# Optimization experiments

Hardware: AMD Instinct MI355X
Metric: run time of the kernel (lower is better)

The kernel has to match this reference:

```python
import jax, jax.numpy as jnp
import numpy as np

B, S, D = 1024, 256, 256  # batch, n_class, feature dim (g = n_component = 1)


def setup_inputs() -> dict:
    key = jax.random.key(0)
    k1, k2, k3 = jax.random.split(key, 3)
    x = jax.random.normal(k1, (B, D), dtype=jnp.float32)
    mu_p = jax.random.normal(k2, (S, 1, D), dtype=jnp.float32)
    sigma_p = jax.random.normal(k3, (S, 1, D, D), dtype=jnp.float32)
    return {"x": x, "mu_p": mu_p, "sigma_p": sigma_p}


def _log_probs(x, mu_p, sigma_p):
    sp = sigma_p[:, 0]            # (S, D, D), component index g=0
    mu = mu_p[:, 0]               # (S, D)
    # parameter_enforcing: m = sigma_p^T @ sigma_p (PSD);
    # mean of (real) eigenvalues of m == trace(m)/D, so the ridge term is
    # 0.01 * (trace(m)/D) * I, making sigma symmetric positive definite.
    m = jnp.einsum('skd,ske->sde', sp, sp)                      # (S, D, D)
    ridge = 0.01 * (jnp.trace(m, axis1=-2, axis2=-1) / D)       # (S,)
    sigma = m + ridge[:, None, None] * jnp.eye(D, dtype=m.dtype)
    # MVN log_prob via Cholesky: logdet = 2*sum(log diag L),
    # maha = || L^{-1} (x - mu) ||^2
    L = jnp.linalg.cholesky(sigma)                              # (S, D, D)
    logdet = 2.0 * jnp.sum(jnp.log(jnp.diagonal(L, axis1=-2, axis2=-1)), -1)  # (S,)
    diff = x[None, :, :] - mu[:, None, :]                       # (S, B, D)
    # batched triangular solve per class: y = L^{-1} diff^T -> (S, D, B)
    y = jax.vmap(lambda Ls, ds: jax.scipy.linalg.solve_triangular(Ls, ds.T, lower=True))(L, diff)
    maha = jnp.sum(y * y, axis=1)                               # (S, B)
    log2pi = jnp.log(2.0 * jnp.pi).astype(x.dtype)
    logp = -0.5 * (D * log2pi + logdet[:, None] + maha)         # (S, B)
    return logp.T                                               # (B, S)


def reference(x, mu_p, sigma_p):
    return _log_probs(x, mu_p, sigma_p)
```

## Files before the change

### kernel.cpp

```cpp
#include <hip/hip_runtime.h>
#include <math.h>


#define LOG2PI_D 470.4965290007924f

typedef __attribute__((ext_vector_type(8))) short bf16x8;
typedef __attribute__((ext_vector_type(4))) float f32x4;

__device__ __forceinline__ unsigned bf16rtn(float f) {
  unsigned u = __float_as_uint(f);
  return (u + 0x7FFFu + ((u >> 16) & 1u)) >> 16;
}
__device__ __forceinline__ unsigned packhl(float v) {
  unsigned h = bf16rtn(v);
  float hf = __uint_as_float(h << 16);
  unsigned l = bf16rtn(v - hf);
  return (h << 16) | l;
}

__global__ __launch_bounds__(256) void k_gram(const float* __restrict__ sp,
                                              float* __restrict__ L,
                                              float* __restrict__ ridge_out) {
  __shared__ unsigned Hb[4 * 128 * 20];
  unsigned* AH = Hb;
  unsigned* AL = Hb + 128 * 20;
  unsigned* BH = Hb + 2 * 128 * 20;
  unsigned* BL = Hb + 3 * 128 * 20;
  int p = blockIdx.y, s = blockIdx.x;
  int bi = (p ? 128 : 0), bj = (p == 2 ? 128 : 0);
  const float* A = sp + (size_t)s * 65536;
  float* C = L + (size_t)s * 65536;
  int tid = threadIdx.x, w = tid >> 6, lane = tid & 63;
  int q = lane >> 4, n = lane & 15;
  int mt_[2] = {w, 7 - w};
  f32x4 acc[2][8] = {};
  int c = tid & 127, g = tid >> 7;

  float va[16], vb[16];
#pragma unroll
  for (int u = 0; u < 16; ++u) {
    va[u] = A[(size_t)(g * 16 + u) * 256 + bi + c];
    if (p == 1) vb[u] = A[(size_t)(g * 16 + u) * 256 + bj + c];
  }

  for (int ks = 0; ks < 8; ++ks) {
    __syncthreads();
    {
      unsigned hw[8], lw[8];
#pragma unroll
      for (int m = 0; m < 8; ++m) {
        float v0 = va[2 * m], v1 = va[2 * m + 1];
        unsigned h0 = bf16rtn(v0), h1 = bf16rtn(v1);
        float r0 = v0 - __uint_as_float(h0 << 16);
        float r1 = v1 - __uint_as_float(h1 << 16);
        hw[m] = h0 | (h1 << 16);
        lw[m] = bf16rtn(r0) | (bf16rtn(r1) << 16);
      }
      *(uint4*)&AH[c * 20 + g * 8] = make_uint4(hw[0], hw[1], hw[2], hw[3]);
      *(uint4*)&AH[c * 20 + g * 8 + 4] = make_uint4(hw[4], hw[5], hw[6], hw[7]);
      *(uint4*)&AL[c * 20 + g * 8] = make_uint4(lw[0], lw[1], lw[2], lw[3]);
      *(uint4*)&AL[c * 20 + g * 8 + 4] = make_uint4(lw[4], lw[5], lw[6], lw[7]);
      if (p == 1) {
#pragma unroll
        for (int m = 0; m < 8; ++m) {
          float v0 = vb[2 * m], v1 = vb[2 * m + 1];
          unsigned h0 = bf16rtn(v0), h1 = bf16rtn(v1);
          float r0 = v0 - __uint_as_float(h0 << 16);
          float r1 = v1 - __uint_as_float(h1 << 16);
          hw[m] = h0 | (h1 << 16);
          lw[m] = bf16rtn(r0) | (bf16rtn(r1) << 16);
        }
        *(uint4*)&BH[c * 20 + g * 8] = make_uint4(hw[0], hw[1], hw[2], hw[3]);
        *(uint4*)&BH[c * 20 + g * 8 + 4] = make_uint4(hw[4], hw[5], hw[6], hw[7]);
        *(uint4*)&BL[c * 20 + g * 8] = make_uint4(lw[0], lw[1], lw[2], lw[3]);
        *(uint4*)&BL[c * 20 + g * 8 + 4] = make_uint4(lw[4], lw[5], lw[6], lw[7]);
      }
    }
    __syncthreads();
    if (ks < 7) {
      int r0g = (ks + 1) * 32 + g * 16;
#pragma unroll
      for (int u = 0; u < 16; ++u) {
        va[u] = A[(size_t)(r0g + u) * 256 + bi + c];
        if (p == 1) vb[u] = A[(size_t)(r0g + u) * 256 + bj + c];
      }
    }
    const unsigned* TBH = (p == 1) ? BH : AH;
    const unsigned* TBL = (p == 1) ? BL : AL;
    bf16x8 Ah[2], Al[2];
#pragma unroll
    for (int t = 0; t < 2; ++t) {
      int col = mt_[t] * 16 + n;
      Ah[t] = *(const bf16x8*)&AH[col * 20 + q * 4];
      Al[t] = *(const bf16x8*)&AL[col * 20 + q * 4];
    }
    int ntmax = (p == 1) ? 8 : (8 - w);
    for (int nt = 0; nt < ntmax; ++nt) {
      bf16x8 bh = *(const bf16x8*)&TBH[(nt * 16 + n) * 20 + q * 4];
      bf16x8 bl = *(const bf16x8*)&TBL[(nt * 16 + n) * 20 + q * 4];
#pragma unroll
      for (int t = 0; t < 2; ++t) {
        if (p == 1 || nt <= mt_[t]) {
          acc[t][nt] = __builtin_amdgcn_mfma_f32_16x16x32_bf16(Ah[t], bh, acc[t][nt], 0, 0, 0);
          acc[t][nt] = __builtin_amdgcn_mfma_f32_16x16x32_bf16(Ah[t], bl, acc[t][nt], 0, 0, 0);
          acc[t][nt] = __builtin_amdgcn_mfma_f32_16x16x32_bf16(Al[t], bh, acc[t][nt], 0, 0, 0);
        }
      }
    }
  }
  if (p != 1) {
    float dsum = 0.f;
#pragma unroll
    for (int t = 0; t < 2; ++t) {
      if ((n >> 2) == q) dsum += acc[t][mt_[t]][n & 3];
    }
    dsum += __shfl_down(dsum, 32, 64);
    dsum += __shfl_down(dsum, 16, 64);
    dsum += __shfl_down(dsum, 8, 64);
    dsum += __shfl_down(dsum, 4, 64);
    dsum += __shfl_down(dsum, 2, 64);
    dsum += __shfl_down(dsum, 1, 64);
    if (lane == 0) atomicAdd(&ridge_out[s], dsum * (0.01f / 256.0f));
  }
  float* slab = (float*)Hb;
  for (int t = 0; t < 2; ++t) {
    __syncthreads();
#pragma unroll
    for (int nt = 0; nt < 8; ++nt)
#pragma unroll
      for (int r = 0; r < 4; ++r)
        slab[w * 2048 + (q * 4 + r) * 128 + nt * 16 + n] = acc[t][nt][r];
    __syncthreads();
#pragma unroll
    for (int it = 0; it < 8; ++it) {
      int idx = tid + it * 256;
      int row = idx >> 5, c4 = idx & 31;
      int wsrc = row >> 4, r16 = row & 15;
      int rt = t ? (7 - wsrc) : wsrc;
      if (p == 1 || (c4 >> 2) <= rt) {
        int d = bi + rt * 16 + r16;
        *(float4*)(C + (size_t)d * 256 + bj + c4 * 4) =
            *(float4*)&slab[wsrc * 2048 + r16 * 128 + c4 * 4];
      }
    }
  }
}

__global__ __launch_bounds__(256) void k_factor(float* __restrict__ L,
                                                const float* __restrict__ ridge_buf) {
  extern __shared__ float lds[];
  float* P = lds;
  float* W = lds + 64 * 68;
  float* WT = lds + 2 * 64 * 68;
  float* T = lds + 3 * 64 * 68;
  int s = blockIdx.x;
  float* M = L + (size_t)s * 65536;
  unsigned* M32 = (unsigned*)M;
  int tid = threadIdx.x;
  int k4 = tid & 15, rb = tid >> 4;
  int ty = tid >> 4, tx = tid & 15;
  float ridge = ridge_buf[s];

  for (int kb = 0; kb < 4; ++kb) {
    int base = kb * 64;
    __syncthreads();
    for (int r = rb; r < 64; r += 16)
      *(float4*)&P[r * 68 + k4 * 4] = *(const float4*)(M + (size_t)(base + r) * 256 + base + k4 * 4);
    __syncthreads();
    if (tid < 64) P[tid * 68 + tid] += ridge;
    __syncthreads();
    {
      int eo = tid & 63, ro = tid >> 6;
      for (int cb = 0; cb < 16; ++cb) {
        int c0 = cb * 4;
        float g00 = P[c0 * 68 + c0];
        float g10 = P[(c0 + 1) * 68 + c0], g11 = P[(c0 + 1) * 68 + c0 + 1];
        float g20 = P[(c0 + 2) * 68 + c0], g21 = P[(c0 + 2) * 68 + c0 + 1],
              g22 = P[(c0 + 2) * 68 + c0 + 2];
        float g30 = P[(c0 + 3) * 68 + c0], g31 = P[(c0 + 3) * 68 + c0 + 1],
              g32 = P[(c0 + 3) * 68 + c0 + 2], g33 = P[(c0 + 3) * 68 + c0 + 3];
        float l00 = sqrtf(g00), r0 = 1.f / l00;
        float l10 = g10 * r0, l20 = g20 * r0, l30 = g30 * r0;
        float l11 = sqrtf(g11 - l10 * l10), r1 = 1.f / l11;
        float l21 = (g21 - l20 * l10) * r1, l31 = (g31 - l30 * l10) * r1;
        float l22 = sqrtf(g22 - l20 * l20 - l21 * l21), r2 = 1.f / l22;
        float l32 = (g32 - l30 * l20 - l31 * l21) * r2;
        float l33 = sqrtf(g33 - l30 * l30 - l31 * l31 - l32 * l32), r3 = 1.f / l33;
        int e = c0 + 4 + eo;
        if (e < 64) {
          float p0 = P[e * 68 + c0], p1 = P[e * 68 + c0 + 1];
          float p2 = P[e * 68 + c0 + 2], p3 = P[e * 68 + c0 + 3];
          float le0 = p0 * r0;
          float le1 = (p1 - le0 * l10) * r1;
          float le2 = (p2 - le0 * l20 - le1 * l21) * r2;
          float le3 = (p3 - le0 * l30 - le1 * l31 - le2 * l32) * r3;
          for (int r = c0 + 4 + ro; r < 64; r += 4) {
            float q0 = P[r * 68 + c0], q1 = P[r * 68 + c0 + 1];
            float q2 = P[r * 68 + c0 + 2], q3 = P[r * 68 + c0 + 3];
            float lr0 = q0 * r0;
            float lr1 = (q1 - lr0 * l10) * r1;
            float lr2 = (q2 - lr0 * l20 - lr1 * l21) * r2;
            float lr3 = (q3 - lr0 * l30 - lr1 * l31 - lr2 * l32) * r3;
            P[r * 68 + e] -= lr0 * le0 + lr1 * le1 + lr2 * le2 + lr3 * le3;
          }
        }
        __syncthreads();
      }
    }
    {
      int cb = tid >> 4, lane16 = tid & 15;
      int c0 = cb * 4;
      float g00 = P[c0 * 68 + c0];
      float g10 = P[(c0 + 1) * 68 + c0], g11 = P[(c0 + 1) * 68 + c0 + 1];
      float g20 = P[(c0 + 2) * 68 + c0], g21 = P[(c0 + 2) * 68 + c0 + 1],
            g22 = P[(c0 + 2) * 68 + c0 + 2];
      float g30 = P[(c0 + 3) * 68 + c0], g31 = P[(c0 + 3) * 68 + c0 + 1],
            g32 = P[(c0 + 3) * 68 + c0 + 2], g33 = P[(c0 + 3) * 68 + c0 + 3];
      float l00 = sqrtf(g00), r0 = 1.f / l00;
      float l10 = g10 * r0, l20 = g20 * r0, l30 = g30 * r0;
      float l11 = sqrtf(g11 - l10 * l10), r1 = 1.f / l11;
      float l21 = (g21 - l20 * l10) * r1, l31 = (g31 - l30 * l10) * r1;
      float l22 = sqrtf(g22 - l20 * l20 - l21 * l21), r2 = 1.f / l22;
      float l32 = (g32 - l30 * l20 - l31 * l21) * r2;
      float l33 = sqrtf(g33 - l30 * l30 - l31 * l31 - l32 * l32), r3 = 1.f / l33;
      float vals[4][4];
      int rows[4], nr = 0;
      for (int r = c0 + lane16; r < 64; r += 16) {
        int i = r - c0;
        if (i == 0) { vals[nr][0] = l00; vals[nr][1] = 0; vals[nr][2] = 0; vals[nr][3] = 0; }
        else if (i == 1) { vals[nr][0] = l10; vals[nr][1] = l11; vals[nr][2] = 0; vals[nr][3] = 0; }
        else if (i == 2) { vals[nr][0] = l20; vals[nr][1] = l21; vals[nr][2] = l22; vals[nr][3] = 0; }
        else if (i == 3) { vals[nr][0] = l30; vals[nr][1] = l31; vals[nr][2] = l32; vals[nr][3] = l33; }
        else {
          float q0 = P[r * 68 + c0], q1 = P[r * 68 + c0 + 1];
          float q2 = P[r * 68 + c0 + 2], q3 = P[r * 68 + c0 + 3];
          float lr0 = q0 * r0;
          float lr1 = (q1 - lr0 * l10) * r1;
          float lr2 = (q2 - lr0 * l20 - lr1 * l21) * r2;
          float lr3 = (q3 - lr0 * l30 - lr1 * l31 - lr2 * l32) * r3;
          vals[nr][0] = lr0; vals[nr][1] = lr1; vals[nr][2] = lr2; vals[nr][3] = lr3;
        }
        rows[nr++] = r;
      }
      __syncthreads();
      for (int u = 0; u < nr; ++u) {
        int r = rows[u];
        P[r * 68 + c0] = vals[u][0];
        P[r * 68 + c0 + 1] = vals[u][1];
        P[r * 68 + c0 + 2] = vals[u][2];
        P[r * 68 + c0 + 3] = vals[u][3];
      }
    }
    __syncthreads();
    if (tid < 64) {
      int c = tid;
      int rl = (c < 32) ? 32 : 64;
      for (int r = 0; r < c; ++r) W[r * 68 + c] = 0.f;
      W[c * 68 + c] = 1.0f / P[c * 68 + c];
      for (int r = c + 1; r < rl; ++r) {
        float a = 0.f;
        for (int k = c; k < r; ++k) a += P[r * 68 + k] * W[k * 68 + c];
        W[r * 68 + c] = -a / P[r * 68 + r];
      }
    }
    __syncthreads();
    {
      int r0 = (tid >> 4) * 2, c0 = (tid & 15) * 2;
      float a00 = 0, a01 = 0, a10 = 0, a11 = 0;
      for (int k = 0; k < 32; ++k) {
        float b0 = P[(32 + r0) * 68 + k], b1 = P[(33 + r0) * 68 + k];
        float w0 = W[k * 68 + c0], w1 = W[k * 68 + c0 + 1];
        a00 += b0 * w0; a01 += b0 * w1; a10 += b1 * w0; a11 += b1 * w1;
      }
      T[r0 * 68 + c0] = a00; T[r0 * 68 + c0 + 1] = a01;
      T[(r0 + 1) * 68 + c0] = a10; T[(r0 + 1) * 68 + c0 + 1] = a11;
    }
    __syncthreads();
    {
      int r0 = (tid >> 4) * 2, c0 = (tid & 15) * 2;
      float a00 = 0, a01 = 0, a10 = 0, a11 = 0;
      for (int k = 0; k < 32; ++k) {
        float i0 = W[(32 + r0) * 68 + 32 + k], i1 = W[(33 + r0) * 68 + 32 + k];
        float t0 = T[k * 68 + c0], t1 = T[k * 68 + c0 + 1];
        a00 += i0 * t0; a01 += i0 * t1; a10 += i1 * t0; a11 += i1 * t1;
      }
      W[(32 + r0) * 68 + c0] = -a00; W[(32 + r0) * 68 + c0 + 1] = -a01;
      W[(33 + r0) * 68 + c0] = -a10; W[(33 + r0) * 68 + c0 + 1] = -a11;
    }
    __syncthreads();
    for (int c = rb; c < 64; c += 16) {
      float4 v = *(float4*)&W[c * 68 + k4 * 4];
      WT[(k4 * 4 + 0) * 68 + c] = v.x;
      WT[(k4 * 4 + 1) * 68 + c] = v.y;
      WT[(k4 * 4 + 2) * 68 + c] = v.z;
      WT[(k4 * 4 + 3) * 68 + c] = v.w;
    }
    __syncthreads();
    for (int r = rb; r < 64; r += 16)
      *(float4*)(M + (size_t)(base + r) * 256 + base + k4 * 4) = *(float4*)&W[r * 68 + k4 * 4];
    int nrt = 3 - kb;
    for (int rt = 0; rt < nrt; ++rt) {
      int g0 = base + 64 + rt * 64;
      __syncthreads();
      for (int r = rb; r < 64; r += 16) {
        float4 v = *(const float4*)(M + (size_t)(g0 + r) * 256 + base + k4 * 4);
        T[(k4 * 4 + 0) * 68 + r] = v.x;
        T[(k4 * 4 + 1) * 68 + r] = v.y;
        T[(k4 * 4 + 2) * 68 + r] = v.z;
        T[(k4 * 4 + 3) * 68 + r] = v.w;
      }
      __syncthreads();
      float acc[4][4] = {};
      for (int k = 0; k < 64; ++k) {
        float a[4], b[4];
        *(float4*)a = *(float4*)&T[k * 68 + ty * 4];
        *(float4*)b = *(float4*)&WT[k * 68 + tx * 4];
#pragma unroll
        for (int i = 0; i < 4; ++i)
#pragma unroll
          for (int j = 0; j < 4; ++j) acc[i][j] += a[i] * b[j];
      }
      __syncthreads();
#pragma unroll
      for (int i = 0; i < 4; ++i)
        *(float4*)(M + (size_t)(g0 + ty * 4 + i) * 256 + base + tx * 4) =
            make_float4(acc[i][0], acc[i][1], acc[i][2], acc[i][3]);
#pragma unroll
      for (int i = 0; i < 4; ++i)
#pragma unroll
        for (int j = 0; j < 4; ++j) T[(tx * 4 + j) * 68 + ty * 4 + i] = acc[i][j];
      __syncthreads();
      for (int r = rb; r < 64; r += 16)
        *(float4*)(M + (size_t)(base + r) * 256 + g0 + k4 * 4) = *(float4*)&T[r * 68 + k4 * 4];
    }
    for (int ti = kb + 1; ti < 4; ++ti) {
      for (int tj = kb + 1; tj <= ti; ++tj) {
        __syncthreads();
        for (int k = rb; k < 64; k += 16) {
          *(float4*)&P[k * 68 + k4 * 4] =
              *(const float4*)(M + (size_t)(base + k) * 256 + ti * 64 + k4 * 4);
          *(float4*)&W[k * 68 + k4 * 4] =
              *(const float4*)(M + (size_t)(base + k) * 256 + tj * 64 + k4 * 4);
        }
        float acc[4][4];
#pragma unroll
        for (int i = 0; i < 4; ++i)
          *(float4*)&acc[i][0] =
              *(const float4*)(M + (size_t)(ti * 64 + ty * 4 + i) * 256 + tj * 64 + tx * 4);
        __syncthreads();
        for (int k = 0; k < 64; ++k) {
          float a[4], b[4];
          *(float4*)a = *(float4*)&P[k * 68 + ty * 4];
          *(float4*)b = *(float4*)&W[k * 68 + tx * 4];
#pragma unroll
          for (int i = 0; i < 4; ++i)
#pragma unroll
            for (int j = 0; j < 4; ++j) acc[i][j] -= a[i] * b[j];
        }
#pragma unroll
        for (int i = 0; i < 4; ++i)
          *(float4*)(M + (size_t)(ti * 64 + ty * 4 + i) * 256 + tj * 64 + tx * 4) =
              make_float4(acc[i][0], acc[i][1], acc[i][2], acc[i][3]);
      }
    }
  }

  {
    float* Bcol = lds;
    float* LW = lds + 3 * 64 * 68;
    float* Cs = LW + 64 * 68;
    for (int j = 0; j < 3; ++j) {
      __syncthreads();
      for (int r = rb; r < 64; r += 16)
        *(float4*)&Bcol[r * 68 + k4 * 4] =
            *(const float4*)(M + (size_t)(j * 64 + r) * 256 + j * 64 + k4 * 4);
      __syncthreads();

      for (int i = j + 1; i < 4; ++i) {
        float acc[4][4] = {};
        for (int kk = j; kk < i; ++kk) {
          __syncthreads();
          for (int k = rb; k < 64; k += 16)
            *(float4*)&LW[k * 68 + k4 * 4] =
                *(const float4*)(M + (size_t)(kk * 64 + k) * 256 + i * 64 + k4 * 4);
          __syncthreads();
          float* Bk = Bcol + (kk - j) * 64 * 68;
#pragma unroll 4
          for (int k = 0; k < 64; ++k) {
            float a[4], b[4];
            *(float4*)a = *(float4*)&LW[k * 68 + ty * 4];
            *(float4*)b = *(float4*)&Bk[k * 68 + tx * 4];
#pragma unroll
            for (int r = 0; r < 4; ++r)
#pragma unroll
              for (int cc = 0; cc < 4; ++cc) acc[r][cc] += a[r] * b[cc];
          }
        }
        __syncthreads();
#pragma unroll
        for (int r = 0; r < 4; ++r)
          *(float4*)&Cs[(ty * 4 + r) * 68 + tx * 4] =
              make_float4(acc[r][0], acc[r][1], acc[r][2], acc[r][3]);
        for (int r = rb; r < 64; r += 16) {
          float4 v = *(const float4*)(M + (size_t)(i * 64 + r) * 256 + i * 64 + k4 * 4);
          LW[(k4 * 4 + 0) * 68 + r] = v.x;
          LW[(k4 * 4 + 1) * 68 + r] = v.y;
          LW[(k4 * 4 + 2) * 68 + r] = v.z;
          LW[(k4 * 4 + 3) * 68 + r] = v.w;
        }
        __syncthreads();
        float d[4][4] = {};
#pragma unroll 4
        for (int k = 0; k < 64; ++k) {
          float a[4], b[4];
          *(float4*)a = *(float4*)&LW[k * 68 + ty * 4];
          *(float4*)b = *(float4*)&Cs[k * 68 + tx * 4];
#pragma unroll
          for (int r = 0; r < 4; ++r)
#pragma unroll
            for (int cc = 0; cc < 4; ++cc) d[r][cc] -= a[r] * b[cc];
        }
        float* Bi = Bcol + (i - j) * 64 * 68;
#pragma unroll
        for (int r = 0; r < 4; ++r) {
          if (i < 3)
            *(float4*)&Bi[(ty * 4 + r) * 68 + tx * 4] =
                make_float4(d[r][0], d[r][1], d[r][2], d[r][3]);
          uint4 pu;
          pu.x = packhl(d[r][0]); pu.y = packhl(d[r][1]);
          pu.z = packhl(d[r][2]); pu.w = packhl(d[r][3]);
          *(uint4*)(M32 + (size_t)(i * 64 + ty * 4 + r) * 256 + j * 64 + tx * 4) = pu;
        }
        __syncthreads();
      }
    }
  }
}

__global__ __launch_bounds__(512) void k_maha(const float* __restrict__ x,
                                              const float* __restrict__ mu_p,
                                              const float* __restrict__ Lw,
                                              float* __restrict__ out) {
  __shared__ __align__(16) short Bh[128 * 40];
  __shared__ __align__(16) short Bl[128 * 40];
  __shared__ float Red[1025];
  int s = blockIdx.x, b0 = blockIdx.y * 128;
  const float* Mf = Lw + (size_t)s * 65536;
  const unsigned* M32 = (const unsigned*)Mf;
  int tid = threadIdx.x, w = tid >> 6, lane = tid & 63;
  int q = lane >> 4, n = lane & 15;
  int mt_[2] = {w, 15 - w};
  f32x4 acc[2][8] = {};

  for (int ks = 0; ks < 8; ++ks) {
    __syncthreads();
    {
      int b = tid >> 2, q8 = tid & 3;
      const float* xp = x + (size_t)(b0 + b) * 256 + ks * 32 + q8 * 8;
      const float* mp = mu_p + (size_t)s * 256 + ks * 32 + q8 * 8;
      float4 xa = ((const float4*)xp)[0], xb = ((const float4*)xp)[1];
      float4 ma = ((const float4*)mp)[0], mb = ((const float4*)mp)[1];
      float dv[8] = {xa.x - ma.x, xa.y - ma.y, xa.z - ma.z, xa.w - ma.w,
                     xb.x - mb.x, xb.y - mb.y, xb.z - mb.z, xb.w - mb.w};
      unsigned h[8], l[8];
#pragma unroll
      for (int jj = 0; jj < 8; ++jj) {
        h[jj] = bf16rtn(dv[jj]);
        float hf = __uint_as_float(h[jj] << 16);
        l[jj] = bf16rtn(dv[jj] - hf);
      }
      *(uint4*)&Bh[b * 40 + q8 * 8] =
          make_uint4(h[0] | (h[1] << 16), h[2] | (h[3] << 16),
                     h[4] | (h[5] << 16), h[6] | (h[7] << 16));
      *(uint4*)&Bl[b * 40 + q8 * 8] =
          make_uint4(l[0] | (l[1] << 16), l[2] | (l[3] << 16),
                     l[4] | (l[5] << 16), l[6] | (l[7] << 16));
    }
    __syncthreads();
    bf16x8 Ah[2], Al[2];
    bool act[2];
#pragma unroll
    for (int t = 0; t < 2; ++t) {
      int mt = mt_[t];
      act[t] = ks < ((mt + 2) >> 1);
      if (act[t]) {
        const unsigned* ap = M32 + (size_t)(mt * 16 + n) * 256 + ks * 32 + q * 8;
        uint4 u0 = *(const uint4*)ap;
        uint4 u1 = *(const uint4*)(ap + 4);
        unsigned uu[8] = {u0.x, u0.y, u0.z, u0.w, u1.x, u1.y, u1.z, u1.w};
        if ((ks >> 1) == (mt >> 2)) {
#pragma unroll
          for (int jj = 0; jj < 8; ++jj) {
            float f = __uint_as_float(uu[jj]);
            unsigned hh = bf16rtn(f);
            float hf = __uint_as_float(hh << 16);
            Ah[t][jj] = (short)hh;
            Al[t][jj] = (short)bf16rtn(f - hf);
          }
        } else {
#pragma unroll
          for (int jj = 0; jj < 8; ++jj) {
            Ah[t][jj] = (short)(uu[jj] >> 16);
            Al[t][jj] = (short)(uu[jj] & 0xffffu);
          }
        }
      }
    }
#pragma unroll
    for (int bsub = 0; bsub < 8; ++bsub) {
      bf16x8 bh = *(const bf16x8*)&Bh[(bsub * 16 + n) * 40 + q * 8];
      bf16x8 bl = *(const bf16x8*)&Bl[(bsub * 16 + n) * 40 + q * 8];
#pragma unroll
      for (int t = 0; t < 2; ++t) {
        if (act[t]) {
          acc[t][bsub] = __builtin_amdgcn_mfma_f32_16x16x32_bf16(Ah[t], bh, acc[t][bsub], 0, 0, 0);
          acc[t][bsub] = __builtin_amdgcn_mfma_f32_16x16x32_bf16(Ah[t], bl, acc[t][bsub], 0, 0, 0);
          acc[t][bsub] = __builtin_amdgcn_mfma_f32_16x16x32_bf16(Al[t], bh, acc[t][bsub], 0, 0, 0);
        }
      }
    }
  }
#pragma unroll
  for (int bsub = 0; bsub < 8; ++bsub) {
    float v = 0.f;
#pragma unroll
    for (int t = 0; t < 2; ++t)
#pragma unroll
      for (int r = 0; r < 4; ++r) v += acc[t][bsub][r] * acc[t][bsub][r];
    v += __shfl_xor(v, 16, 64);
    v += __shfl_xor(v, 32, 64);
    if (lane < 16) Red[w * 128 + bsub * 16 + lane] = v;
  }
  if (w == 0) {
    float ld = 0.f;
#pragma unroll
    for (int c = 0; c < 4; ++c)
      ld += logf(Mf[(size_t)(c * 64 + lane) * 256 + c * 64 + lane]);
    ld += __shfl_down(ld, 32, 64);
    ld += __shfl_down(ld, 16, 64);
    ld += __shfl_down(ld, 8, 64);
    ld += __shfl_down(ld, 4, 64);
    ld += __shfl_down(ld, 2, 64);
    ld += __shfl_down(ld, 1, 64);
    if (lane == 0) Red[1024] = ld;
  }
  __syncthreads();
  if (tid < 128) {
    float mh = 0.f;
#pragma unroll
    for (int w2 = 0; w2 < 8; ++w2) mh += Red[w2 * 128 + tid];
    out[(size_t)(b0 + tid) * 256 + s] = -0.5f * (LOG2PI_D - 2.0f * Red[1024] + mh);
  }
}

extern "C" void kernel_launch(void* const* d_in, const int* in_sizes, int n_in,
                              void* d_out, int out_size, void* d_ws, size_t ws_size,
                              hipStream_t stream) {
  const float* x = (const float*)d_in[0];
  const float* mu = (const float*)d_in[1];
  const float* sp = (const float*)d_in[2];
  float* out = (float*)d_out;
  float* L = (float*)d_ws;

  const int fact_lds = 5 * 64 * 68 * 4;
  (void)hipFuncSetAttribute((const void*)k_factor,
                            hipFuncAttributeMaxDynamicSharedMemorySize, fact_lds);

  k_gram<<<dim3(256, 3), 256, 0, stream>>>(sp, L, out);
  k_factor<<<256, 256, fact_lds, stream>>>(L, out);
  k_maha<<<dim3(256, 8), 512, 0, stream>>>(x, mu, L, out);
}
```

Measured before the change: 654.7 us.

## Double factor kernel block size and process two trailing tiles concurrently

Raises k_factor to 512 threads per block. The two thread halves now process pairs of panel and trailing-update tiles in parallel, using an extra LDS buffer. The diagonal-block triangular inverse changes from a serial per-column loop on 64 threads to a blocked 4-row forward substitution driven by a 256-thread partial-sum step. The intent is to raise per-block parallelism in the serial Cholesky phase, at the cost of idle threads in some phases, extra barriers and higher register pressure.

New measurement: 614.7 us. 6.1% less time.

```diff
diff --git a/kernel.cpp b/kernel.cpp
--- a/kernel.cpp
+++ b/kernel.cpp
@@ -146,19 +146,19 @@
   }
 }
 
-__global__ __launch_bounds__(256) void k_factor(float* __restrict__ L,
+__global__ __launch_bounds__(512) void k_factor(float* __restrict__ L,
                                                 const float* __restrict__ ridge_buf) {
   extern __shared__ float lds[];
   float* P = lds;
   float* W = lds + 64 * 68;
   float* WT = lds + 2 * 64 * 68;
   float* T = lds + 3 * 64 * 68;
+  float* T2 = lds + 4 * 64 * 68;
   int s = blockIdx.x;
   float* M = L + (size_t)s * 65536;
   unsigned* M32 = (unsigned*)M;
   int tid = threadIdx.x;
   int k4 = tid & 15, rb = tid >> 4;
-  int ty = tid >> 4, tx = tid & 15;
   float ridge = ridge_buf[s];
 
   for (int kb = 0; kb < 4; ++kb) {
@@ -194,7 +194,7 @@
           float le1 = (p1 - le0 * l10) * r1;
           float le2 = (p2 - le0 * l20 - le1 * l21) * r2;
           float le3 = (p3 - le0 * l30 - le1 * l31 - le2 * l32) * r3;
-          for (int r = c0 + 4 + ro; r < 64; r += 4) {
+          for (int r = c0 + 4 + ro; r < 64; r += 8) {
             float q0 = P[r * 68 + c0], q1 = P[r * 68 + c0 + 1];
             float q2 = P[r * 68 + c0 + 2], q3 = P[r * 68 + c0 + 3];
             float lr0 = q0 * r0;
@@ -210,84 +210,85 @@
     {
       int cb = tid >> 4, lane16 = tid & 15;
       int c0 = cb * 4;
-      float g00 = P[c0 * 68 + c0];
-      float g10 = P[(c0 + 1) * 68 + c0], g11 = P[(c0 + 1) * 68 + c0 + 1];
-      float g20 = P[(c0 + 2) * 68 + c0], g21 = P[(c0 + 2) * 68 + c0 + 1],
-            g22 = P[(c0 + 2) * 68 + c0 + 2];
-      float g30 = P[(c0 + 3) * 68 + c0], g31 = P[(c0 + 3) * 68 + c0 + 1],
-            g32 = P[(c0 + 3) * 68 + c0 + 2], g33 = P[(c0 + 3) * 68 + c0 + 3];
-      float l00 = sqrtf(g00), r0 = 1.f / l00;
-      float l10 = g10 * r0, l20 = g20 * r0, l30 = g30 * r0;
-      float l11 = sqrtf(g11 - l10 * l10), r1 = 1.f / l11;
-      float l21 = (g21 - l20 * l10) * r1, l31 = (g31 - l30 * l10) * r1;
-      float l22 = sqrtf(g22 - l20 * l20 - l21 * l21), r2 = 1.f / l22;
-      float l32 = (g32 - l30 * l20 - l31 * l21) * r2;
-      float l33 = sqrtf(g33 - l30 * l30 - l31 * l31 - l32 * l32), r3 = 1.f / l33;
       float vals[4][4];
       int rows[4], nr = 0;
-      for (int r = c0 + lane16; r < 64; r += 16) {
-        int i = r - c0;
-        if (i == 0) { vals[nr][0] = l00; vals[nr][1] = 0; vals[nr][2] = 0; vals[nr][3] = 0; }
-        else if (i == 1) { vals[nr][0] = l10; vals[nr][1] = l11; vals[nr][2] = 0; vals[nr][3] = 0; }
-        else if (i == 2) { vals[nr][0] = l20; vals[nr][1] = l21; vals[nr][2] = l22; vals[nr][3] = 0; }
-        else if (i == 3) { vals[nr][0] = l30; vals[nr][1] = l31; vals[nr][2] = l32; vals[nr][3] = l33; }
-        else {
-          float q0 = P[r * 68 + c0], q1 = P[r * 68 + c0 + 1];
-          float q2 = P[r * 68 + c0 + 2], q3 = P[r * 68 + c0 + 3];
-          float lr0 = q0 * r0;
-          float lr1 = (q1 - lr0 * l10) * r1;
-          float lr2 = (q2 - lr0 * l20 - lr1 * l21) * r2;
-          float lr3 = (q3 - lr0 * l30 - lr1 * l31 - lr2 * l32) * r3;
-          vals[nr][0] = lr0; vals[nr][1] = lr1; vals[nr][2] = lr2; vals[nr][3] = lr3;
-        }
-        rows[nr++] = r;
-      }
-      __syncthreads();
-      for (int u = 0; u < nr; ++u) {
-        int r = rows[u];
-        P[r * 68 + c0] = vals[u][0];
-        P[r * 68 + c0 + 1] = vals[u][1];
-        P[r * 68 + c0 + 2] = vals[u][2];
-        P[r * 68 + c0 + 3] = vals[u][3];
-      }
-    }
-    __syncthreads();
-    if (tid < 64) {
-      int c = tid;
-      int rl = (c < 32) ? 32 : 64;
-      for (int r = 0; r < c; ++r) W[r * 68 + c] = 0.f;
-      W[c * 68 + c] = 1.0f / P[c * 68 + c];
-      for (int r = c + 1; r < rl; ++r) {
-        float a = 0.f;
-        for (int k = c; k < r; ++k) a += P[r * 68 + k] * W[k * 68 + c];
-        W[r * 68 + c] = -a / P[r * 68 + r];
-      }
-    }
-    __syncthreads();
-    {
-      int r0 = (tid >> 4) * 2, c0 = (tid & 15) * 2;
-      float a00 = 0, a01 = 0, a10 = 0, a11 = 0;
-      for (int k = 0; k < 32; ++k) {
-        float b0 = P[(32 + r0) * 68 + k], b1 = P[(33 + r0) * 68 + k];
-        float w0 = W[k * 68 + c0], w1 = W[k * 68 + c0 + 1];
-        a00 += b0 * w0; a01 += b0 * w1; a10 += b1 * w0; a11 += b1 * w1;
-      }
-      T[r0 * 68 + c0] = a00; T[r0 * 68 + c0 + 1] = a01;
-      T[(r0 + 1) * 68 + c0] = a10; T[(r0 + 1) * 68 + c0 + 1] = a11;
-    }
-    __syncthreads();
-    {
-      int r0 = (tid >> 4) * 2, c0 = (tid & 15) * 2;
-      float a00 = 0, a01 = 0, a10 = 0, a11 = 0;
-      for (int k = 0; k < 32; ++k) {
-        float i0 = W[(32 + r0) * 68 + 32 + k], i1 = W[(33 + r0) * 68 + 32 + k];
-        float t0 = T[k * 68 + c0], t1 = T[k * 68 + c0 + 1];
-        a00 += i0 * t0; a01 += i0 * t1; a10 += i1 * t0; a11 += i1 * t1;
-      }
-      W[(32 + r0) * 68 + c0] = -a00; W[(32 + r0) * 68 + c0 + 1] = -a01;
-      W[(33 + r0) * 68 + c0] = -a10; W[(33 + r0) * 68 + c0 + 1] = -a11;
-    }
-    __syncthreads();
+      if (tid < 256) {
+        float g00 = P[c0 * 68 + c0];
+        float g10 = P[(c0 + 1) * 68 + c0], g11 = P[(c0 + 1) * 68 + c0 + 1];
+        float g20 = P[(c0 + 2) * 68 + c0], g21 = P[(c0 + 2) * 68 + c0 + 1],
+              g22 = P[(c0 + 2) * 68 + c0 + 2];
+        float g30 = P[(c0 + 3) * 68 + c0], g31 = P[(c0 + 3) * 68 + c0 + 1],
+              g32 = P[(c0 + 3) * 68 + c0 + 2], g33 = P[(c0 + 3) * 68 + c0 + 3];
+        float l00 = sqrtf(g00), r0 = 1.f / l00;
+        float l10 = g10 * r0, l20 = g20 * r0, l30 = g30 * r0;
+        float l11 = sqrtf(g11 - l10 * l10), r1 = 1.f / l11;
+        float l21 = (g21 - l20 * l10) * r1, l31 = (g31 - l30 * l10) * r1;
+        float l22 = sqrtf(g22 - l20 * l20 - l21 * l21), r2 = 1.f / l22;
+        float l32 = (g32 - l30 * l20 - l31 * l21) * r2;
+        float l33 = sqrtf(g33 - l30 * l30 - l31 * l31 - l32 * l32), r3 = 1.f / l33;
+        for (int r = c0 + lane16; r < 64; r += 16) {
+          int i = r - c0;
+          if (i == 0) { vals[nr][0] = l00; vals[nr][1] = 0; vals[nr][2] = 0; vals[nr][3] = 0; }
+          else if (i == 1) { vals[nr][0] = l10; vals[nr][1] = l11; vals[nr][2] = 0; vals[nr][3] = 0; }
+          else if (i == 2) { vals[nr][0] = l20; vals[nr][1] = l21; vals[nr][2] = l22; vals[nr][3] = 0; }
+          else if (i == 3) { vals[nr][0] = l30; vals[nr][1] = l31; vals[nr][2] = l32; vals[nr][3] = l33; }
+          else {
+            float q0 = P[r * 68 + c0], q1 = P[r * 68 + c0 + 1];
+            float q2 = P[r * 68 + c0 + 2], q3 = P[r * 68 + c0 + 3];
+            float lr0 = q0 * r0;
+            float lr1 = (q1 - lr0 * l10) * r1;
+            float lr2 = (q2 - lr0 * l20 - lr1 * l21) * r2;
+            float lr3 = (q3 - lr0 * l30 - lr1 * l31 - lr2 * l32) * r3;
+            vals[nr][0] = lr0; vals[nr][1] = lr1; vals[nr][2] = lr2; vals[nr][3] = lr3;
+          }
+          rows[nr++] = r;
+        }
+      }
+      __syncthreads();
+      if (tid < 256) {
+        for (int u = 0; u < nr; ++u) {
+          int r = rows[u];
+          P[r * 68 + c0] = vals[u][0];
+          P[r * 68 + c0 + 1] = vals[u][1];
+          P[r * 68 + c0 + 2] = vals[u][2];
+          P[r * 68 + c0 + 3] = vals[u][3];
+        }
+      }
+    }
+    __syncthreads();
+    for (int idx = tid; idx < 64 * 68; idx += 512) W[idx] = 0.f;
+    __syncthreads();
+    for (int rb4 = 0; rb4 < 16; ++rb4) {
+      int k0 = rb4 * 4;
+      if (tid < 256) {
+        int i = tid >> 6, cc = tid & 63;
+        int row = k0 + i;
+        float ssum = 0.f;
+        for (int k = 0; k < k0; ++k) ssum += P[row * 68 + k] * W[k * 68 + cc];
+        WT[i * 68 + cc] = ssum;
+      }
+      __syncthreads();
+      if (tid < 64) {
+        int cc = tid;
+        float d00 = P[(k0 + 0) * 68 + k0];
+        float d10 = P[(k0 + 1) * 68 + k0], d11 = P[(k0 + 1) * 68 + k0 + 1];
+        float d20 = P[(k0 + 2) * 68 + k0], d21 = P[(k0 + 2) * 68 + k0 + 1],
+              d22 = P[(k0 + 2) * 68 + k0 + 2];
+        float d30 = P[(k0 + 3) * 68 + k0], d31 = P[(k0 + 3) * 68 + k0 + 1],
+              d32 = P[(k0 + 3) * 68 + k0 + 2], d33 = P[(k0 + 3) * 68 + k0 + 3];
+        float e0 = (cc == k0) ? 1.f : 0.f, e1 = (cc == k0 + 1) ? 1.f : 0.f;
+        float e2 = (cc == k0 + 2) ? 1.f : 0.f, e3 = (cc == k0 + 3) ? 1.f : 0.f;
+        float x0 = (e0 - WT[0 * 68 + cc]) / d00;
+        float x1 = (e1 - WT[1 * 68 + cc] - d10 * x0) / d11;
+        float x2 = (e2 - WT[2 * 68 + cc] - d20 * x0 - d21 * x1) / d22;
+        float x3 = (e3 - WT[3 * 68 + cc] - d30 * x0 - d31 * x1 - d32 * x2) / d33;
+        W[(k0 + 0) * 68 + cc] = x0;
+        W[(k0 + 1) * 68 + cc] = x1;
+        W[(k0 + 2) * 68 + cc] = x2;
+        W[(k0 + 3) * 68 + cc] = x3;
+      }
+      __syncthreads();
+    }
     for (int c = rb; c < 64; c += 16) {
       float4 v = *(float4*)&W[c * 68 + k4 * 4];
       WT[(k4 * 4 + 0) * 68 + c] = v.x;
@@ -299,59 +300,92 @@
     for (int r = rb; r < 64; r += 16)
       *(float4*)(M + (size_t)(base + r) * 256 + base + k4 * 4) = *(float4*)&W[r * 68 + k4 * 4];
     int nrt = 3 - kb;
-    for (int rt = 0; rt < nrt; ++rt) {
-      int g0 = base + 64 + rt * 64;
-      __syncthreads();
-      for (int r = rb; r < 64; r += 16) {
-        float4 v = *(const float4*)(M + (size_t)(g0 + r) * 256 + base + k4 * 4);
-        T[(k4 * 4 + 0) * 68 + r] = v.x;
-        T[(k4 * 4 + 1) * 68 + r] = v.y;
-        T[(k4 * 4 + 2) * 68 + r] = v.z;
-        T[(k4 * 4 + 3) * 68 + r] = v.w;
+    for (int rt0 = 0; rt0 < nrt; rt0 += 2) {
+      int pr = tid >> 8, t2 = tid & 255;
+      int my = rt0 + pr;
+      bool act = my < nrt;
+      float* Tb = pr ? T2 : T;
+      int k42 = t2 & 15, rb2 = t2 >> 4;
+      int ty2 = t2 >> 4, tx2 = t2 & 15;
+      int g0 = base + 64 + my * 64;
+      __syncthreads();
+      if (act) {
+        for (int r = rb2; r < 64; r += 16) {
+          float4 v = *(const float4*)(M + (size_t)(g0 + r) * 256 + base + k42 * 4);
+          Tb[(k42 * 4 + 0) * 68 + r] = v.x;
+          Tb[(k42 * 4 + 1) * 68 + r] = v.y;
+          Tb[(k42 * 4 + 2) * 68 + r] = v.z;
+          Tb[(k42 * 4 + 3) * 68 + r] = v.w;
+        }
       }
       __syncthreads();
       float acc[4][4] = {};
-      for (int k = 0; k < 64; ++k) {
-        float a[4], b[4];
-        *(float4*)a = *(float4*)&T[k * 68 + ty * 4];
-        *(float4*)b = *(float4*)&WT[k * 68 + tx * 4];
+      if (act) {
+        for (int k = 0; k < 64; ++k) {
+          float a[4], b[4];
+          *(float4*)a = *(float4*)&Tb[k * 68 + ty2 * 4];
+          *(float4*)b = *(float4*)&WT[k * 68 + tx2 * 4];
+#pragma unroll
+          for (int i = 0; i < 4; ++i)
+#pragma unroll
+            for (int j = 0; j < 4; ++j) acc[i][j] += a[i] * b[j];
+        }
+      }
+      __syncthreads();
+      if (act) {
 #pragma unroll
         for (int i = 0; i < 4; ++i)
-#pragma unroll
-          for (int j = 0; j < 4; ++j) acc[i][j] += a[i] * b[j];
-      }
-      __syncthreads();
-#pragma unroll
-      for (int i = 0; i < 4; ++i)
-        *(float4*)(M + (size_t)(g0 + ty * 4 + i) * 256 + base + tx * 4) =
-            make_float4(acc[i][0], acc[i][1], acc[i][2], acc[i][3]);
-#pragma unroll
-      for (int i = 0; i < 4; ++i)
-#pragma unroll
-        for (int j = 0; j < 4; ++j) T[(tx * 4 + j) * 68 + ty * 4 + i] = acc[i][j];
-      __syncthreads();
-      for (int r = rb; r < 64; r += 16)
-        *(float4*)(M + (size_t)(base + r) * 256 + g0 + k4 * 4) = *(float4*)&T[r * 68 + k4 * 4];
-    }
-    for (int ti = kb + 1; ti < 4; ++ti) {
-      for (int tj = kb + 1; tj <= ti; ++tj) {
-        __syncthreads();
-        for (int k = rb; k < 64; k += 16) {
-          *(float4*)&P[k * 68 + k4 * 4] =
-              *(const float4*)(M + (size_t)(base + k) * 256 + ti * 64 + k4 * 4);
-          *(float4*)&W[k * 68 + k4 * 4] =
-              *(const float4*)(M + (size_t)(base + k) * 256 + tj * 64 + k4 * 4);
-        }
-        float acc[4][4];
+          *(float4*)(M + (size_t)(g0 + ty2 * 4 + i) * 256 + base + tx2 * 4) =
+              make_float4(acc[i][0], acc[i][1], acc[i][2], acc[i][3]);
+#pragma unroll
+        for (int i = 0; i < 4; ++i)
+#pragma unroll
+          for (int j = 0; j < 4; ++j) Tb[(tx2 * 4 + j) * 68 + ty2 * 4 + i] = acc[i][j];
+      }
+      __syncthreads();
+      if (act) {
+        for (int r = rb2; r < 64; r += 16)
+          *(float4*)(M + (size_t)(base + r) * 256 + g0 + k42 * 4) = *(float4*)&Tb[r * 68 + k42 * 4];
+      }
+    }
+    int np = ((3 - kb) * (4 - kb)) / 2;
+    for (int p0 = 0; p0 < np; p0 += 2) {
+      int pr = tid >> 8, t2 = tid & 255;
+      int my = p0 + pr;
+      bool act = my < np;
+      int ti = 1, tj = 1;
+      {
+        int cnt = 0;
+        for (int a = kb + 1; a < 4; ++a)
+          for (int b = kb + 1; b <= a; ++b) {
+            if (cnt == my) { ti = a; tj = b; }
+            ++cnt;
+          }
+      }
+      float* Pi = pr ? WT : P;
+      float* Pj = pr ? T : W;
+      int k42 = t2 & 15, rb2 = t2 >> 4;
+      int ty2 = t2 >> 4, tx2 = t2 & 15;
+      __syncthreads();
+      float acc[4][4];
+      if (act) {
+        for (int k = rb2; k < 64; k += 16) {
+          *(float4*)&Pi[k * 68 + k42 * 4] =
+              *(const float4*)(M + (size_t)(base + k) * 256 + ti * 64 + k42 * 4);
+          *(float4*)&Pj[k * 68 + k42 * 4] =
+              *(const float4*)(M + (size_t)(base + k) * 256 + tj * 64 + k42 * 4);
+        }
 #pragma unroll
         for (int i = 0; i < 4; ++i)
           *(float4*)&acc[i][0] =
-              *(const float4*)(M + (size_t)(ti * 64 + ty * 4 + i) * 256 + tj * 64 + tx * 4);
-        __syncthreads();
+              *(const float4*)(M + (size_t)(ti * 64 + ty2 * 4 + i) * 256 + tj * 64 + tx2 * 4);
+      }
+      __syncthreads();
+      if (act) {
         for (int k = 0; k < 64; ++k) {
           float a[4], b[4];
-          *(float4*)a = *(float4*)&P[k * 68 + ty * 4];
-          *(float4*)b = *(float4*)&W[k * 68 + tx * 4];
+          *(float4*)a = *(float4*)&Pi[k * 68 + ty2 * 4];
+          *(float4*)b = *(float4*)&Pj[k * 68 + tx2 * 4];
 #pragma unroll
           for (int i = 0; i < 4; ++i)
 #pragma unroll
@@ -359,7 +393,7 @@
         }
 #pragma unroll
         for (int i = 0; i < 4; ++i)
-          *(float4*)(M + (size_t)(ti * 64 + ty * 4 + i) * 256 + tj * 64 + tx * 4) =
+          *(float4*)(M + (size_t)(ti * 64 + ty2 * 4 + i) * 256 + tj * 64 + tx2 * 4) =
               make_float4(acc[i][0], acc[i][1], acc[i][2], acc[i][3]);
       }
     }
@@ -368,7 +402,8 @@
   {
     float* Bcol = lds;
     float* LW = lds + 3 * 64 * 68;
-    float* Cs = LW + 64 * 68;
+    float* Cs = lds + 4 * 64 * 68;
+    int ty = tid >> 4, tx = tid & 15;
     for (int j = 0; j < 3; ++j) {
       __syncthreads();
       for (int r = rb; r < 64; r += 16)
@@ -385,22 +420,26 @@
                 *(const float4*)(M + (size_t)(kk * 64 + k) * 256 + i * 64 + k4 * 4);
           __syncthreads();
           float* Bk = Bcol + (kk - j) * 64 * 68;
+          if (tid < 256) {
 #pragma unroll 4
-          for (int k = 0; k < 64; ++k) {
-            float a[4], b[4];
-            *(float4*)a = *(float4*)&LW[k * 68 + ty * 4];
-            *(float4*)b = *(float4*)&Bk[k * 68 + tx * 4];
-#pragma unroll
-            for (int r = 0; r < 4; ++r)
-#pragma unroll
-              for (int cc = 0; cc < 4; ++cc) acc[r][cc] += a[r] * b[cc];
+            for (int k = 0; k < 64; ++k) {
+              float a[4], b[4];
+              *(float4*)a = *(float4*)&LW[k * 68 + ty * 4];
+              *(float4*)b = *(float4*)&Bk[k * 68 + tx * 4];
+#pragma unroll
+              for (int r = 0; r < 4; ++r)
+#pragma unroll
+                for (int cc = 0; cc < 4; ++cc) acc[r][cc] += a[r] * b[cc];
+            }
           }
         }
         __syncthreads();
-#pragma unroll
-        for (int r = 0; r < 4; ++r)
-          *(float4*)&Cs[(ty * 4 + r) * 68 + tx * 4] =
-              make_float4(acc[r][0], acc[r][1], acc[r][2], acc[r][3]);
+        if (tid < 256) {
+#pragma unroll
+          for (int r = 0; r < 4; ++r)
+            *(float4*)&Cs[(ty * 4 + r) * 68 + tx * 4] =
+                make_float4(acc[r][0], acc[r][1], acc[r][2], acc[r][3]);
+        }
         for (int r = rb; r < 64; r += 16) {
           float4 v = *(const float4*)(M + (size_t)(i * 64 + r) * 256 + i * 64 + k4 * 4);
           LW[(k4 * 4 + 0) * 68 + r] = v.x;
@@ -409,27 +448,29 @@
           LW[(k4 * 4 + 3) * 68 + r] = v.w;
         }
         __syncthreads();
-        float d[4][4] = {};
+        if (tid < 256) {
+          float d[4][4] = {};
 #pragma unroll 4
-        for (int k = 0; k < 64; ++k) {
-          float a[4], b[4];
-          *(float4*)a = *(float4*)&LW[k * 68 + ty * 4];
-          *(float4*)b = *(float4*)&Cs[k * 68 + tx * 4];
-#pragma unroll
-          for (int r = 0; r < 4; ++r)
-#pragma unroll
-            for (int cc = 0; cc < 4; ++cc) d[r][cc] -= a[r] * b[cc];
-        }
-        float* Bi = Bcol + (i - j) * 64 * 68;
-#pragma unroll
-        for (int r = 0; r < 4; ++r) {
-          if (i < 3)
-            *(float4*)&Bi[(ty * 4 + r) * 68 + tx * 4] =
-                make_float4(d[r][0], d[r][1], d[r][2], d[r][3]);
-          uint4 pu;
-          pu.x = packhl(d[r][0]); pu.y = packhl(d[r][1]);
-          pu.z = packhl(d[r][2]); pu.w = packhl(d[r][3]);
-          *(uint4*)(M32 + (size_t)(i * 64 + ty * 4 + r) * 256 + j * 64 + tx * 4) = pu;
+          for (int k = 0; k < 64; ++k) {
+            float a[4], b[4];
+            *(float4*)a = *(float4*)&LW[k * 68 + ty * 4];
+            *(float4*)b = *(float4*)&Cs[k * 68 + tx * 4];
+#pragma unroll
+            for (int r = 0; r < 4; ++r)
+#pragma unroll
+              for (int cc = 0; cc < 4; ++cc) d[r][cc] -= a[r] * b[cc];
+          }
+          float* Bi = Bcol + (i - j) * 64 * 68;
+#pragma unroll
+          for (int r = 0; r < 4; ++r) {
+            if (i < 3)
+              *(float4*)&Bi[(ty * 4 + r) * 68 + tx * 4] =
+                  make_float4(d[r][0], d[r][1], d[r][2], d[r][3]);
+            uint4 pu;
+            pu.x = packhl(d[r][0]); pu.y = packhl(d[r][1]);
+            pu.z = packhl(d[r][2]); pu.w = packhl(d[r][3]);
+            *(uint4*)(M32 + (size_t)(i * 64 + ty * 4 + r) * 256 + j * 64 + tx * 4) = pu;
+          }
         }
         __syncthreads();
       }
@@ -567,6 +608,6 @@
                             hipFuncAttributeMaxDynamicSharedMemorySize, fact_lds);
 
   k_gram<<<dim3(256, 3), 256, 0, stream>>>(sp, L, out);
-  k_factor<<<256, 256, fact_lds, stream>>>(L, out);
+  k_factor<<<256, 512, fact_lds, stream>>>(L, out);
   k_maha<<<dim3(256, 8), 512, 0, stream>>>(x, mu, L, out);
 }
```
